# Performance work log

Hardware: AMD Instinct MI355X
Metric: run time of the kernel (lower is better)

The kernel has to match this reference:

```python
import jax, jax.numpy as jnp
import numpy as np

HEADS = 16
DIM_HEAD = 64


def setup_inputs() -> dict:
    key = jax.random.key(0)
    k1, k2, k3, k4, k5 = jax.random.split(key, 5)
    B, L, D = 8, 4096, 1024
    hidden = HEADS * DIM_HEAD  # 1024
    x = jax.random.normal(k1, (B, L, D), dtype=jnp.float32)
    masks = jax.random.randint(k2, (B, L), 0, 2).astype(bool)
    w_qkv = jax.random.normal(k3, (3 * hidden, D), dtype=jnp.float32) * (D ** -0.5)
    w_out = jax.random.normal(k4, (D, hidden), dtype=jnp.float32) * (hidden ** -0.5)
    b_out = jax.random.normal(k5, (D,), dtype=jnp.float32) * 0.01
    return {"x": x, "masks": masks, "w_qkv": w_qkv, "w_out": w_out, "b_out": b_out}


def reference(x, masks, w_qkv, w_out, b_out):
    B, L, D = x.shape
    H, d = HEADS, DIM_HEAD
    scale = d ** -0.5
    # x -> [B, D, L]; zero out masked tokens
    xt = jnp.where(masks[:, None, :], 0.0, x.transpose(0, 2, 1))
    # 1x1 conv == channel matmul: [B, 3*H*d, L]
    qkv = jnp.einsum('od,bdl->bol', w_qkv, xt)
    q, k, v = jnp.split(qkv, 3, axis=1)
    q = q.reshape(B, H, d, L) * scale
    k = k.reshape(B, H, d, L)
    v = v.reshape(B, H, d, L)
    m = masks[:, None, None, :]  # [B,1,1,L]
    q = jnp.where(m, 0.0, q)
    k = jnp.where(m, -1e15, k)
    k = jax.nn.softmax(k, axis=-1)
    # context = k @ v^T : [B,H,d,d]
    context = jnp.einsum('bhdl,bhel->bhde', k, v)
    # out = context @ q : [B,H,d,L]
    out = jnp.einsum('bhde,bhel->bhdl', context, q)
    out = out.reshape(B, H * d, L)
    out = jnp.einsum('oc,bcl->bol', w_out, out) + b_out[None, :, None]
    return out.transpose(0, 2, 1)  # [B, L, D]
```

## Files before the change

### kernel.cpp

```cpp
#include <hip/hip_runtime.h>
#include <hip/hip_bf16.h>
#include <stdint.h>

typedef __attribute__((ext_vector_type(8))) short short8;
typedef __attribute__((ext_vector_type(4))) float floatx4;
typedef unsigned short u16;

#define MFMA(a,b,c) __builtin_amdgcn_mfma_f32_16x16x32_bf16(a,b,c,0,0,0)

__device__ __forceinline__ u16 f2bf(float f) {
  __hip_bfloat16 h = __float2bfloat16(f);
  return *reinterpret_cast<u16*>(&h);
}
__device__ __forceinline__ float bf2f(u16 u) {
  union { uint32_t i; float f; } v; v.i = ((uint32_t)u) << 16; return v.f;
}

__device__ __forceinline__ void gload16(const void* g, void* l) {
  __builtin_amdgcn_global_load_lds(
      (__attribute__((address_space(1))) void*)(uintptr_t)g,
      (__attribute__((address_space(3))) void*)l, 16, 0, 0);
}

__global__ void k_maskcvt(const float* __restrict__ x, const int* __restrict__ masks,
                          u16* __restrict__ xm) {
  int gid = blockIdx.x * blockDim.x + threadIdx.x;
  size_t i8 = (size_t)gid * 8;
  int row = gid >> 7;
  int msk = masks[row];
  float4 v0 = make_float4(0.f,0.f,0.f,0.f), v1 = v0;
  if (!msk) {
    v0 = *(const float4*)(x + i8);
    v1 = *(const float4*)(x + i8 + 4);
  }
  ushort4 p0 = make_ushort4(f2bf(v0.x), f2bf(v0.y), f2bf(v0.z), f2bf(v0.w));
  ushort4 p1 = make_ushort4(f2bf(v1.x), f2bf(v1.y), f2bf(v1.z), f2bf(v1.w));
  *(ushort4*)(xm + i8) = p0;
  *(ushort4*)(xm + i8 + 4) = p1;
}

__global__ void k_cvt(const float* __restrict__ s, u16* __restrict__ d) {
  int gid = blockIdx.x * blockDim.x + threadIdx.x;
  size_t i8 = (size_t)gid * 8;
  float4 v0 = *(const float4*)(s + i8);
  float4 v1 = *(const float4*)(s + i8 + 4);
  ushort4 p0 = make_ushort4(f2bf(v0.x), f2bf(v0.y), f2bf(v0.z), f2bf(v0.w));
  ushort4 p1 = make_ushort4(f2bf(v1.x), f2bf(v1.y), f2bf(v1.z), f2bf(v1.w));
  *(ushort4*)(d + i8) = p0;
  *(ushort4*)(d + i8 + 4) = p1;
}

__global__ __launch_bounds__(256) void k_cvtT(const float* __restrict__ src,
                                              u16* __restrict__ dst) {
  __shared__ float t[32][33];
  const int e0 = blockIdx.x * 32, c0 = blockIdx.y * 32;
  const int tx = threadIdx.x & 31, ty = threadIdx.x >> 5;
  #pragma unroll
  for (int i = 0; i < 4; i++)
    t[ty + i*8][tx] = src[(size_t)(e0 + ty + i*8) * 1024 + c0 + tx];
  __syncthreads();
  #pragma unroll
  for (int i = 0; i < 4; i++)
    dst[(size_t)(c0 + ty + i*8) * 1024 + e0 + tx] = f2bf(t[tx][ty + i*8] * 0.125f);
}

template<int MODE>
__global__ __launch_bounds__(256) void gemm_bt(
    const u16* __restrict__ A, const u16* __restrict__ Bm,
    u16* __restrict__ o_k, u16* __restrict__ o_v,
    u16* __restrict__ o_mb,
    float* __restrict__ outp, const float* __restrict__ bias) {
  constexpr int K = 1024;
  __shared__ u16 As[128*32];
  __shared__ u16 Bs[128*32];
  const int tid = threadIdx.x;
  const int lane = tid & 63, w = tid >> 6;
  const int wr = w >> 1, wc = w & 1;
  const int lrow = lane & 15, lk = lane >> 4;

  int m_idx, n_idx, zb = 0;
  if (MODE == 0) {
    int id = blockIdx.x, j = id >> 3;
    m_idx = j & 15; n_idx = (id & 7) * 32 + (j >> 4);
  } else if (MODE == 1) {
    int id = blockIdx.x, j = id >> 3;
    n_idx = j & 7; m_idx = (id & 7) * 32 + (j >> 3);
  } else {
    m_idx = blockIdx.x & 7; n_idx = blockIdx.x >> 3; zb = blockIdx.z;
  }
  const int m0 = m_idx * 128, n0 = n_idx * 128;

  const u16* Ap = A + (size_t)m0 * K;
  const u16* Bp;
  if (MODE == 1)      Bp = Bm + (size_t)(m0 >> 12) * 1048576 + (size_t)n0 * K;
  else if (MODE == 2) Bp = Bm + (size_t)zb * 1048576 + (size_t)n0 * K;
  else                Bp = Bm + (size_t)n0 * K;

  floatx4 acc[4][4] = {};

  for (int k0 = 0; k0 < K; k0 += 32) {
    #pragma unroll
    for (int r = 0; r < 2; ++r) {
      int li = r*256 + tid;
      int row = li >> 2, seg = li & 3;
      gload16(Ap + (size_t)row * K + k0 + seg*8, (char*)As + (r*256 + w*64)*16);
      gload16(Bp + (size_t)row * K + k0 + seg*8, (char*)Bs + (r*256 + w*64)*16);
    }
    __syncthreads();
    short8 af[4], bff[4];
    #pragma unroll
    for (int m=0;m<4;m++) af[m]  = *(const short8*)&As[(wr*64 + m*16 + lrow)*32 + lk*8];
    #pragma unroll
    for (int n=0;n<4;n++) bff[n] = *(const short8*)&Bs[(wc*64 + n*16 + lrow)*32 + lk*8];
    #pragma unroll
    for (int m=0;m<4;m++)
      #pragma unroll
      for (int n=0;n<4;n++)
        acc[m][n] = MFMA(af[m], bff[n], acc[m][n]);
    __syncthreads();
  }

  #pragma unroll
  for (int m=0;m<4;m++) {
    const int rbase = m0 + wr*64 + m*16;
    #pragma unroll
    for (int n=0;n<4;n++) {
      const int ocol = n0 + wc*64 + n*16 + lrow;
      floatx4 d = acc[m][n];
      if (MODE == 0) {
        const int b = ocol >> 12, l = ocol & 4095;
        if (rbase < 1024) {
          int orow = rbase + lk*4;
          #pragma unroll
          for (int r=0;r<4;r++)
            o_k[((size_t)b*1024 + orow + r)*4096 + l] = f2bf(d[r]);
        } else {
          int orow = rbase - 1024 + lk*4;
          #pragma unroll
          for (int r=0;r<4;r++)
            o_v[((size_t)b*1024 + orow + r)*4096 + l] = f2bf(d[r]);
        }
      } else if (MODE == 1) {
        int orow = rbase + lk*4;
        float bval = bias[ocol];
        #pragma unroll
        for (int r=0;r<4;r++)
          outp[(size_t)(orow + r)*1024 + ocol] = d[r] + bval;
      } else {
        int orow = rbase + lk*4;
        #pragma unroll
        for (int r=0;r<4;r++)
          o_mb[(size_t)zb*1048576 + (size_t)(orow + r)*1024 + ocol] = f2bf(d[r]);
      }
    }
  }
}

__global__ __launch_bounds__(256) void k_softmax(u16* __restrict__ kbf,
    const int* __restrict__ masks) {
  const int row = blockIdx.x;
  const int b = row >> 10;
  u16* src = kbf + (size_t)row * 4096;
  const int* mk = masks + (size_t)b * 4096;
  const int tid = threadIdx.x;
  const int lane = tid & 63, wv = tid >> 6;

  float v[16]; int mv[16];
  float mx = -INFINITY;
  #pragma unroll
  for (int i=0;i<4;i++) {
    int l = i*1024 + tid*4;
    ushort4 kv = *(const ushort4*)(src + l);
    int4 mm = *(const int4*)(mk + l);
    float f0=bf2f(kv.x), f1=bf2f(kv.y), f2=bf2f(kv.z), f3=bf2f(kv.w);
    v[i*4+0]=f0; v[i*4+1]=f1; v[i*4+2]=f2; v[i*4+3]=f3;
    mv[i*4+0]=mm.x; mv[i*4+1]=mm.y; mv[i*4+2]=mm.z; mv[i*4+3]=mm.w;
    if (!mm.x) mx = fmaxf(mx, f0);
    if (!mm.y) mx = fmaxf(mx, f1);
    if (!mm.z) mx = fmaxf(mx, f2);
    if (!mm.w) mx = fmaxf(mx, f3);
  }
  #pragma unroll
  for (int o=32;o;o>>=1) mx = fmaxf(mx, __shfl_xor(mx, o));
  __shared__ float sred[4];
  __shared__ float ssum[4];
  if (lane==0) sred[wv] = mx;
  __syncthreads();
  mx = fmaxf(fmaxf(sred[0],sred[1]), fmaxf(sred[2],sred[3]));

  float s = 0.f;
  #pragma unroll
  for (int i=0;i<16;i++) {
    float e = mv[i] ? 0.f : __expf(v[i]-mx);
    v[i] = e; s += e;
  }
  #pragma unroll
  for (int o=32;o;o>>=1) s += __shfl_xor(s, o);
  if (lane==0) ssum[wv] = s;
  __syncthreads();
  s = ssum[0]+ssum[1]+ssum[2]+ssum[3];
  float inv = 1.f/s;
  #pragma unroll
  for (int i=0;i<4;i++) {
    int l = i*1024 + tid*4;
    ushort4 p = make_ushort4(f2bf(v[i*4]*inv), f2bf(v[i*4+1]*inv),
                             f2bf(v[i*4+2]*inv), f2bf(v[i*4+3]*inv));
    *(ushort4*)(src + l) = p;
  }
}

__global__ __launch_bounds__(256) void k_context(const u16* __restrict__ ksm,
    const u16* __restrict__ vv, u16* __restrict__ ctx) {
  const int bh = blockIdx.x;
  const int tid = threadIdx.x, lane = tid&63, w = tid>>6;
  const int lrow = lane&15, lk = lane>>4;
  const u16* Kb = ksm + (size_t)bh*64*4096;
  const u16* Vb = vv  + (size_t)bh*64*4096;
  floatx4 acc[4][4] = {};
  const int kbeg = w*1024;
  for (int kk=0; kk<1024; kk+=32) {
    short8 af[4], bff[4];
    #pragma unroll
    for (int m=0;m<4;m++) af[m]  = *(const short8*)(Kb + (size_t)(m*16+lrow)*4096 + kbeg+kk + lk*8);
    #pragma unroll
    for (int n=0;n<4;n++) bff[n] = *(const short8*)(Vb + (size_t)(n*16+lrow)*4096 + kbeg+kk + lk*8);
    #pragma unroll
    for (int m=0;m<4;m++)
      #pragma unroll
      for (int n=0;n<4;n++)
        acc[m][n] = MFMA(af[m], bff[n], acc[m][n]);
  }
  __shared__ float red[4][4096];
  #pragma unroll
  for (int m=0;m<4;m++)
    #pragma unroll
    for (int n=0;n<4;n++)
      #pragma unroll
      for (int r=0;r<4;r++) {
        int dd = m*16 + lk*4 + r, ee = n*16 + lrow;
        red[w][dd*64+ee] = acc[m][n][r];
      }
  __syncthreads();
  u16* cb = ctx + (size_t)bh*4096;
  #pragma unroll
  for (int i=0;i<16;i++) {
    int idx = i*256 + tid;
    cb[idx] = f2bf(red[0][idx]+red[1][idx]+red[2][idx]+red[3][idx]);
  }
}

__global__ __launch_bounds__(256) void k_vb(const u16* __restrict__ ctx,
    const u16* __restrict__ wqT, u16* __restrict__ vbT) {
  const int b = blockIdx.z, h = blockIdx.y, n0 = blockIdx.x * 256;
  const int tid = threadIdx.x, lane = tid & 63, wv = tid >> 6;
  const int lrow = lane & 15, lk = lane >> 4;
  const u16* Cb = ctx + (size_t)(b*16 + h) * 4096;
  floatx4 acc[4][4] = {};
  #pragma unroll
  for (int kk = 0; kk < 64; kk += 32) {
    short8 af[4], bff[4];
    #pragma unroll
    for (int m=0;m<4;m++) af[m]  = *(const short8*)(Cb + (m*16 + lrow)*64 + kk + lk*8);
    #pragma unroll
    for (int n=0;n<4;n++) bff[n] = *(const short8*)(wqT + (size_t)(n0 + wv*64 + n*16 + lrow)*1024 + h*64 + kk + lk*8);
    #pragma unroll
    for (int m=0;m<4;m++)
      #pragma unroll
      for (int n=0;n<4;n++)
        acc[m][n] = MFMA(af[m], bff[n], acc[m][n]);
  }
  u16* dst = vbT + (size_t)b * 1048576;
  #pragma unroll
  for (int m=0;m<4;m++)
    #pragma unroll
    for (int n=0;n<4;n++)
      #pragma unroll
      for (int r=0;r<4;r++) {
        int c = n0 + wv*64 + n*16 + lrow;
        int dd = m*16 + lk*4 + r;
        dst[(size_t)c*1024 + h*64 + dd] = f2bf(acc[m][n][r]);
      }
}

extern "C" void kernel_launch(void* const* d_in, const int* in_sizes, int n_in,
                              void* d_out, int out_size, void* d_ws, size_t ws_size,
                              hipStream_t stream) {
  const float* x     = (const float*)d_in[0];
  const int*   masks = (const int*)d_in[1];
  const float* w_qkv = (const float*)d_in[2];
  const float* w_out = (const float*)d_in[3];
  const float* b_out = (const float*)d_in[4];
  float* out = (float*)d_out;

  char* ws = (char*)d_ws;
  u16* xm  = (u16*)(ws);
  u16* wkv = (u16*)(ws + (64ull<<20));
  u16* wqT = (u16*)(ws + (68ull<<20));
  u16* wob = (u16*)(ws + (70ull<<20));
  u16* ctx = (u16*)(ws + (72ull<<20));
  u16* vbT = (u16*)(ws + (73ull<<20));
  u16* mb  = (u16*)(ws + (89ull<<20));

  u16* kbf = (u16*)d_out;
  u16* vv  = (u16*)d_out + 33554432ull;

  k_maskcvt<<<16384, 256, 0, stream>>>(x, masks, xm);
  k_cvt<<<1024, 256, 0, stream>>>(w_qkv + 1048576, wkv);
  k_cvt<<<512, 256, 0, stream>>>(w_out, wob);
  k_cvtT<<<dim3(32,32), 256, 0, stream>>>(w_qkv, wqT);

  gemm_bt<0><<<4096, 256, 0, stream>>>(wkv, xm, kbf, vv, nullptr, nullptr, nullptr);
  k_softmax<<<8192, 256, 0, stream>>>(kbf, masks);
  k_context<<<128, 256, 0, stream>>>(kbf, vv, ctx);
  k_vb<<<dim3(4,16,8), 256, 0, stream>>>(ctx, wqT, vbT);
  gemm_bt<2><<<dim3(64,1,8), 256, 0, stream>>>(wob, vbT, nullptr, nullptr, mb, nullptr, nullptr);
  gemm_bt<1><<<2048, 256, 0, stream>>>(xm, mb, nullptr, nullptr, nullptr, out, b_out);
}
```

Measured before the change: 567.4 us.

## Use 256x256 double-buffered swizzled GEMM kernel for the two large projections

Adds a 512-thread GEMM kernel with 256x256 output tiles, a K-step of 64, double-buffered LDS fed by global_load_lds, an XOR swizzle against bank conflicts, and s_setprio around the MFMA bursts. It replaces the 128x128 single-buffered kernel for the K/V projection and the final output projection, aiming for more reuse per loaded byte and overlap of the next tile's loads with compute. The small per-batch GEMM stays on the old kernel, now specialised to that mode. The larger LDS footprint (128 KB) and register use mean fewer resident blocks per CU.

```diff
diff --git a/kernel.cpp b/kernel.cpp
--- a/kernel.cpp
+++ b/kernel.cpp
@@ -65,11 +65,121 @@
 }
 
 template<int MODE>
+__global__ __launch_bounds__(512) void gemm256(
+    const u16* __restrict__ A, const u16* __restrict__ Bm,
+    u16* __restrict__ o_k, u16* __restrict__ o_v,
+    float* __restrict__ outp, const float* __restrict__ bias) {
+  constexpr int K = 1024, NT = 16;
+  __shared__ u16 As[2][16384];
+  __shared__ u16 Bs[2][16384];
+  const int tid = threadIdx.x, lane = tid & 63, w = tid >> 6;
+  const int wr = w >> 2, wc = w & 3;
+  const int lrow = lane & 15, lk = lane >> 4;
+
+  int m_idx, n_idx;
+  if (MODE == 0) { int id = blockIdx.x, j = id >> 3; m_idx = j & 7;  n_idx = (id & 7) * 16 + (j >> 3); }
+  else           { int id = blockIdx.x, j = id >> 3; n_idx = j & 3;  m_idx = (id & 7) * 16 + (j >> 2); }
+  const int m0 = m_idx * 256, n0 = n_idx * 256;
+
+  const u16* Ap = A + (size_t)m0 * K;
+  const u16* Bp = (MODE == 1) ? Bm + (size_t)(m0 >> 12) * 1048576 + (size_t)n0 * K
+                              : Bm + (size_t)n0 * K;
+
+  floatx4 acc[8][4] = {};
+
+  auto STAGE = [&](int buf, int t) {
+    const int k0 = t * 64;
+    #pragma unroll
+    for (int i = 0; i < 4; i++) {
+      int li = i * 512 + tid;
+      int row = li >> 3, s = li & 7;
+      int slot = s ^ (row & 7);
+      gload16(Ap + (size_t)row * K + k0 + slot * 8,
+              (char*)&As[buf][0] + (i * 512 + w * 64) * 16);
+    }
+    #pragma unroll
+    for (int i = 0; i < 4; i++) {
+      int li = i * 512 + tid;
+      int row = li >> 3, s = li & 7;
+      int slot = s ^ (row & 7);
+      gload16(Bp + (size_t)row * K + k0 + slot * 8,
+              (char*)&Bs[buf][0] + (i * 512 + w * 64) * 16);
+    }
+  };
+
+  STAGE(0, 0);
+  for (int t = 0; t < NT; ++t) {
+    const int buf = t & 1;
+    if (t + 1 < NT) {
+      STAGE(buf ^ 1, t + 1);
+      asm volatile("s_waitcnt vmcnt(8)" ::: "memory");
+    } else {
+      asm volatile("s_waitcnt vmcnt(0)" ::: "memory");
+    }
+    __builtin_amdgcn_s_barrier();
+    asm volatile("" ::: "memory");
+    const int swz = lrow & 7;
+    #pragma unroll
+    for (int ks = 0; ks < 2; ++ks) {
+      short8 af[8], bf4[4];
+      #pragma unroll
+      for (int m = 0; m < 8; m++) {
+        int r = wr * 128 + m * 16 + lrow;
+        af[m] = *(const short8*)&As[buf][r * 64 + (((ks * 4 + lk) ^ swz) << 3)];
+      }
+      #pragma unroll
+      for (int n = 0; n < 4; n++) {
+        int r = wc * 64 + n * 16 + lrow;
+        bf4[n] = *(const short8*)&Bs[buf][r * 64 + (((ks * 4 + lk) ^ swz) << 3)];
+      }
+      __builtin_amdgcn_s_setprio(1);
+      #pragma unroll
+      for (int m = 0; m < 8; m++)
+        #pragma unroll
+        for (int n = 0; n < 4; n++)
+          acc[m][n] = MFMA(af[m], bf4[n], acc[m][n]);
+      __builtin_amdgcn_s_setprio(0);
+    }
+    asm volatile("" ::: "memory");
+    __builtin_amdgcn_s_barrier();
+    asm volatile("" ::: "memory");
+  }
+
+  #pragma unroll
+  for (int m = 0; m < 8; m++) {
+    const int rbase = m0 + wr * 128 + m * 16;
+    #pragma unroll
+    for (int n = 0; n < 4; n++) {
+      const int ocol = n0 + wc * 64 + n * 16 + lrow;
+      floatx4 d = acc[m][n];
+      if (MODE == 0) {
+        const int b = ocol >> 12, l = ocol & 4095;
+        if (rbase < 1024) {
+          int orow = rbase + lk * 4;
+          #pragma unroll
+          for (int r = 0; r < 4; r++)
+            o_k[((size_t)b * 1024 + orow + r) * 4096 + l] = f2bf(d[r]);
+        } else {
+          int orow = rbase - 1024 + lk * 4;
+          #pragma unroll
+          for (int r = 0; r < 4; r++)
+            o_v[((size_t)b * 1024 + orow + r) * 4096 + l] = f2bf(d[r]);
+        }
+      } else {
+        int orow = rbase + lk * 4;
+        float bval = bias[ocol];
+        #pragma unroll
+        for (int r = 0; r < 4; r++)
+          outp[(size_t)(orow + r) * 1024 + ocol] = d[r] + bval;
+      }
+    }
+  }
+}
+
+template<int MODE>
 __global__ __launch_bounds__(256) void gemm_bt(
     const u16* __restrict__ A, const u16* __restrict__ Bm,
-    u16* __restrict__ o_k, u16* __restrict__ o_v,
-    u16* __restrict__ o_mb,
-    float* __restrict__ outp, const float* __restrict__ bias) {
+    u16* __restrict__ o_mb) {
   constexpr int K = 1024;
   __shared__ u16 As[128*32];
   __shared__ u16 Bs[128*32];
@@ -78,23 +188,11 @@
   const int wr = w >> 1, wc = w & 1;
   const int lrow = lane & 15, lk = lane >> 4;
 
-  int m_idx, n_idx, zb = 0;
-  if (MODE == 0) {
-    int id = blockIdx.x, j = id >> 3;
-    m_idx = j & 15; n_idx = (id & 7) * 32 + (j >> 4);
-  } else if (MODE == 1) {
-    int id = blockIdx.x, j = id >> 3;
-    n_idx = j & 7; m_idx = (id & 7) * 32 + (j >> 3);
-  } else {
-    m_idx = blockIdx.x & 7; n_idx = blockIdx.x >> 3; zb = blockIdx.z;
-  }
+  const int m_idx = blockIdx.x & 7, n_idx = blockIdx.x >> 3, zb = blockIdx.z;
   const int m0 = m_idx * 128, n0 = n_idx * 128;
 
   const u16* Ap = A + (size_t)m0 * K;
-  const u16* Bp;
-  if (MODE == 1)      Bp = Bm + (size_t)(m0 >> 12) * 1048576 + (size_t)n0 * K;
-  else if (MODE == 2) Bp = Bm + (size_t)zb * 1048576 + (size_t)n0 * K;
-  else                Bp = Bm + (size_t)n0 * K;
+  const u16* Bp = Bm + (size_t)zb * 1048576 + (size_t)n0 * K;
 
   floatx4 acc[4][4] = {};
 
@@ -127,31 +225,10 @@
     for (int n=0;n<4;n++) {
       const int ocol = n0 + wc*64 + n*16 + lrow;
       floatx4 d = acc[m][n];
-      if (MODE == 0) {
-        const int b = ocol >> 12, l = ocol & 4095;
-        if (rbase < 1024) {
-          int orow = rbase + lk*4;
-          #pragma unroll
-          for (int r=0;r<4;r++)
-            o_k[((size_t)b*1024 + orow + r)*4096 + l] = f2bf(d[r]);
-        } else {
-          int orow = rbase - 1024 + lk*4;
-          #pragma unroll
-          for (int r=0;r<4;r++)
-            o_v[((size_t)b*1024 + orow + r)*4096 + l] = f2bf(d[r]);
-        }
-      } else if (MODE == 1) {
-        int orow = rbase + lk*4;
-        float bval = bias[ocol];
-        #pragma unroll
-        for (int r=0;r<4;r++)
-          outp[(size_t)(orow + r)*1024 + ocol] = d[r] + bval;
-      } else {
-        int orow = rbase + lk*4;
-        #pragma unroll
-        for (int r=0;r<4;r++)
-          o_mb[(size_t)zb*1048576 + (size_t)(orow + r)*1024 + ocol] = f2bf(d[r]);
-      }
+      int orow = rbase + lk*4;
+      #pragma unroll
+      for (int r=0;r<4;r++)
+        o_mb[(size_t)zb*1048576 + (size_t)(orow + r)*1024 + ocol] = f2bf(d[r]);
     }
   }
 }
@@ -309,10 +386,10 @@
   k_cvt<<<512, 256, 0, stream>>>(w_out, wob);
   k_cvtT<<<dim3(32,32), 256, 0, stream>>>(w_qkv, wqT);
 
-  gemm_bt<0><<<4096, 256, 0, stream>>>(wkv, xm, kbf, vv, nullptr, nullptr, nullptr);
+  gemm256<0><<<1024, 512, 0, stream>>>(wkv, xm, kbf, vv, nullptr, nullptr);
   k_softmax<<<8192, 256, 0, stream>>>(kbf, masks);
   k_context<<<128, 256, 0, stream>>>(kbf, vv, ctx);
   k_vb<<<dim3(4,16,8), 256, 0, stream>>>(ctx, wqT, vbT);
-  gemm_bt<2><<<dim3(64,1,8), 256, 0, stream>>>(wob, vbT, nullptr, nullptr, mb, nullptr, nullptr);
-  gemm_bt<1><<<2048, 256, 0, stream>>>(xm, mb, nullptr, nullptr, nullptr, out, b_out);
-}
+  gemm_bt<2><<<dim3(64,1,8), 256, 0, stream>>>(wob, vbT, mb);
+  gemm256<1><<<512, 512, 0, stream>>>(xm, mb, nullptr, nullptr, out, b_out);
+}
```

Result: faster. 548.6 us (-3.3%).
